# Performance work log

Measured on AMD Instinct MI355X. Metric: run time of the kernel, lower is better.

The kernel has to match this reference:

```python
import jax, jax.numpy as jnp
import numpy as np

B, C, L = 8, 1024, 4096
CTX = 768
NUM_GROUPS = 8
EPS = 1e-5
HEAD_DIM = C  # num_heads = 1 (only shape-consistent config of the module)


def setup_inputs() -> dict:
    key = jax.random.key(0)
    ks = jax.random.split(key, 8)
    s = 0.02
    return {
        "x": jax.random.normal(ks[0], (B, C, L), jnp.float32),
        "context": jax.random.normal(ks[1], (B, CTX), jnp.float32),
        "gn_gamma": jnp.ones((C,), jnp.float32),
        "gn_beta": jnp.zeros((C,), jnp.float32),
        "ln_gamma": jnp.ones((CTX,), jnp.float32),
        "ln_beta": jnp.zeros((CTX,), jnp.float32),
        "Wq": jax.random.normal(ks[2], (C, C), jnp.float32) * s,
        "bq": jnp.zeros((C,), jnp.float32),
        "Wkv": jax.random.normal(ks[3], (2 * C, CTX), jnp.float32) * s,
        "bkv": jnp.zeros((2 * C,), jnp.float32),
        "Wp": jax.random.normal(ks[4], (C, C), jnp.float32) * s,
        "bp": jnp.zeros((C,), jnp.float32),
    }


def group_norm(x, gamma, beta):
    # x: (B, C, L) -> normalize within each of NUM_GROUPS groups over (C//G, L)
    b, c, l = x.shape
    xg = x.reshape(b, NUM_GROUPS, c // NUM_GROUPS, l)
    mu = xg.mean(axis=(2, 3), keepdims=True)
    var = xg.var(axis=(2, 3), keepdims=True)
    xg = (xg - mu) * jax.lax.rsqrt(var + EPS)
    return xg.reshape(b, c, l) * gamma[None, :, None] + beta[None, :, None]


def layer_norm(x, gamma, beta):
    mu = x.mean(axis=-1, keepdims=True)
    var = x.var(axis=-1, keepdims=True)
    return (x - mu) * jax.lax.rsqrt(var + EPS) * gamma + beta


def reference(x, context, gn_gamma, gn_beta, ln_gamma, ln_beta,
              Wq, bq, Wkv, bkv, Wp, bp):
    residual = x
    xn = group_norm(x, gn_gamma, gn_beta)                   # (B, C, L)
    ctx = layer_norm(context, ln_gamma, ln_beta)            # (B, CTX)
    # 1x1 conv Q projection == channel GEMM
    q = jnp.einsum('bcl,oc->bol', xn, Wq) + bq[None, :, None]  # (B, C, L)
    kv = ctx @ Wkv.T + bkv                                  # (B, 2C)
    k, v = kv[:, :C], kv[:, C:]                             # each (B, C) = (B, head_dim)
    scale = HEAD_DIM ** (-0.5)
    # per-position score against the single context key; softmax over L
    attn = jax.nn.softmax(jnp.einsum('bcl,bc->bl', q, k) * scale, axis=-1)  # (B, L)
    # broadcast-weighted outer product (fused form of expand+mul+sum over heads=1)
    out = attn[:, None, :] * v[:, :, None]                  # (B, C, L)
    out = jnp.einsum('bcl,oc->bol', out, Wp) + bp[None, :, None]
    return residual + out
```

## Files before the change

kernel.cpp:

```cpp
#include <hip/hip_runtime.h>
#include <math.h>

#define NB   8
#define NC   1024
#define NL   4096
#define NCTX 768
#define EPSV 1e-5f
#define SCALEV 0.03125f

typedef float floatx4 __attribute__((ext_vector_type(4)));

enum : int {
  OFF_KV    = 0,
  OFF_PV    = 16384,
  OFF_QP    = 24576,
  OFF_SPART = 548864,
  OFF_TPART = 552960,
  OFF_ATTN  = 1077248,
  OFF_S     = 1110016,
  WS_FLOATS = 1110024
};

__device__ __forceinline__ float breduce_sum(float v, float* red) {
  int t = threadIdx.x;
  red[t] = v; __syncthreads();
  for (int s = 128; s > 0; s >>= 1) { if (t < s) red[t] += red[t + s]; __syncthreads(); }
  float r = red[0]; __syncthreads();
  return r;
}
__device__ __forceinline__ float wave_sum(float v) {
  #pragma unroll
  for (int off = 32; off > 0; off >>= 1) v += __shfl_xor(v, off, 64);
  return v;
}

__global__ void k_kv(const float* __restrict__ ctx, const float* __restrict__ lng,
                     const float* __restrict__ lnb, const float* __restrict__ Wkv,
                     const float* __restrict__ bkv, float* __restrict__ ws) {
  __shared__ __align__(16) float scf[8 * NCTX];
  int t = threadIdx.x, bid = blockIdx.x;
  int wave = t >> 6, lane = t & 63;
  if (bid == 0 && t < NB) ws[OFF_S + t] = 0.f;
  #pragma unroll
  for (int bb = 0; bb < 2; bb++) {
    int b = wave * 2 + bb;
    const float* row = ctx + b * NCTX;
    float v[12];
    float s = 0.f;
    #pragma unroll
    for (int k = 0; k < 12; k++) { v[k] = row[lane + 64 * k]; s += v[k]; }
    float mu = wave_sum(s) * (1.0f / NCTX);
    float s2 = 0.f;
    #pragma unroll
    for (int k = 0; k < 12; k++) { float d = v[k] - mu; s2 = fmaf(d, d, s2); }
    float rstd = rsqrtf(wave_sum(s2) * (1.0f / NCTX) + EPSV);
    #pragma unroll
    for (int k = 0; k < 12; k++) {
      int j = lane + 64 * k;
      scf[b * NCTX + j] = (v[k] - mu) * rstd * lng[j] + lnb[j];
    }
  }
  __syncthreads();
  const float4* W4 = reinterpret_cast<const float4*>(Wkv);
  const float4* sc4 = reinterpret_cast<const float4*>(scf);
  #pragma unroll
  for (int rr = 0; rr < 4; rr++) {
    int j = bid * 16 + wave * 4 + rr;
    float4 wv0 = W4[(size_t)j * 192 + lane];
    float4 wv1 = W4[(size_t)j * 192 + lane + 64];
    float4 wv2 = W4[(size_t)j * 192 + lane + 128];
    #pragma unroll
    for (int b = 0; b < 8; b++) {
      const float4* sb = sc4 + b * 192;
      float4 c0 = sb[lane], c1 = sb[lane + 64], c2 = sb[lane + 128];
      float a = wv0.x*c0.x + wv0.y*c0.y + wv0.z*c0.z + wv0.w*c0.w
              + wv1.x*c1.x + wv1.y*c1.y + wv1.z*c1.z + wv1.w*c1.w
              + wv2.x*c2.x + wv2.y*c2.y + wv2.z*c2.z + wv2.w*c2.w;
      a = wave_sum(a);
      if (lane == 0) ws[OFF_KV + b * 2048 + j] = a + bkv[j];
    }
  }
}

__global__ void k_mv(const float* __restrict__ Wq, const float* __restrict__ Wp,
                     float* __restrict__ ws) {
  __shared__ float4 sbuf[8 * 256];
  int t = threadIdx.x, bid = blockIdx.x;
  if (bid < 64) {
    float* sk = reinterpret_cast<float*>(sbuf);
    if (t < 128) { int b = t >> 4, o = t & 15; sk[b * 16 + o] = ws[OFF_KV + b * 2048 + bid * 16 + o]; }
    __syncthreads();
    const float4* Wq4 = reinterpret_cast<const float4*>(Wq);
    float4 acc[8];
    #pragma unroll
    for (int b = 0; b < 8; b++) acc[b] = make_float4(0.f, 0.f, 0.f, 0.f);
    int o0 = bid * 16;
    #pragma unroll 4
    for (int oi = 0; oi < 16; oi++) {
      float4 w = Wq4[(size_t)(o0 + oi) * 256 + t];
      #pragma unroll
      for (int b = 0; b < 8; b++) {
        float kk = sk[b * 16 + oi];
        acc[b].x = fmaf(kk, w.x, acc[b].x);
        acc[b].y = fmaf(kk, w.y, acc[b].y);
        acc[b].z = fmaf(kk, w.z, acc[b].z);
        acc[b].w = fmaf(kk, w.w, acc[b].w);
      }
    }
    float4* qp4 = reinterpret_cast<float4*>(ws + OFF_QP);
    #pragma unroll
    for (int b = 0; b < 8; b++) qp4[(bid * 8 + b) * 256 + t] = acc[b];
  } else {
    const float4* kv4 = reinterpret_cast<const float4*>(ws + OFF_KV);
    #pragma unroll
    for (int rep = 0; rep < 8; rep++) {
      int idx = rep * 256 + t;
      int b = idx >> 8, i = idx & 255;
      sbuf[idx] = kv4[b * 512 + 256 + i];
    }
    __syncthreads();
    int wave = t >> 6, lane = t & 63;
    const float4* Wp4 = reinterpret_cast<const float4*>(Wp);
    #pragma unroll
    for (int rr = 0; rr < 4; rr++) {
      int o = (bid - 64) * 16 + wave * 4 + rr;
      float4 wv0 = Wp4[(size_t)o * 256 + lane];
      float4 wv1 = Wp4[(size_t)o * 256 + lane + 64];
      float4 wv2 = Wp4[(size_t)o * 256 + lane + 128];
      float4 wv3 = Wp4[(size_t)o * 256 + lane + 192];
      #pragma unroll
      for (int b = 0; b < 8; b++) {
        const float4* sb = sbuf + b * 256;
        float4 c0 = sb[lane], c1 = sb[lane + 64], c2 = sb[lane + 128], c3 = sb[lane + 192];
        float a = wv0.x*c0.x + wv0.y*c0.y + wv0.z*c0.z + wv0.w*c0.w
                + wv1.x*c1.x + wv1.y*c1.y + wv1.z*c1.z + wv1.w*c1.w
                + wv2.x*c2.x + wv2.y*c2.y + wv2.z*c2.z + wv2.w*c2.w
                + wv3.x*c3.x + wv3.y*c3.y + wv3.z*c3.z + wv3.w*c3.w;
        a = wave_sum(a);
        if (lane == 0) ws[OFF_PV + b * NC + o] = a;
      }
    }
  }
}

__global__ void k_pass1(const float* __restrict__ x, const float* __restrict__ gng,
                        float* __restrict__ ws) {
  __shared__ float red[256];
  __shared__ float sw[64];
  __shared__ __align__(16) float4 part[192];
  int t  = threadIdx.x;
  int lc = blockIdx.x;
  int cs = blockIdx.y;
  int bz = blockIdx.z;
  int b = bz >> 3, g = bz & 7;
  int c0 = g * 128 + cs * 64;
  {
    int cl = t & 63, sp = t >> 6;
    const float* qp = ws + OFF_QP + b * 1024 + c0 + cl;
    float s = 0.f;
    #pragma unroll 4
    for (int oc = sp * 16; oc < sp * 16 + 16; oc++) s += qp[(size_t)oc * 8192];
    red[t] = s;
    __syncthreads();
    if (t < 64) sw[t] = gng[c0 + t] * ((red[t] + red[t + 64]) + (red[t + 128] + red[t + 192]));
    __syncthreads();
  }
  int tl = t & 63, q = t >> 6;
  int l4 = lc * 64 + tl;
  const float4* x4 = reinterpret_cast<const float4*>(x);
  float4 tacc = make_float4(0.f, 0.f, 0.f, 0.f);
  float s1 = 0.f, s2 = 0.f;
  #pragma unroll 4
  for (int ci = q * 16; ci < q * 16 + 16; ci++) {
    float w = sw[ci];
    float4 v = x4[(size_t)(b * NC + c0 + ci) * 1024 + l4];
    tacc.x = fmaf(w, v.x, tacc.x);
    tacc.y = fmaf(w, v.y, tacc.y);
    tacc.z = fmaf(w, v.z, tacc.z);
    tacc.w = fmaf(w, v.w, tacc.w);
    s1 += (v.x + v.y) + (v.z + v.w);
    s2 = fmaf(v.x, v.x, s2); s2 = fmaf(v.y, v.y, s2);
    s2 = fmaf(v.z, v.z, s2); s2 = fmaf(v.w, v.w, s2);
  }
  if (q > 0) part[(q - 1) * 64 + tl] = tacc;
  __syncthreads();
  if (q == 0) {
    float4 p0 = part[tl], p1 = part[64 + tl], p2 = part[128 + tl];
    tacc.x += (p0.x + p1.x) + p2.x;
    tacc.y += (p0.y + p1.y) + p2.y;
    tacc.z += (p0.z + p1.z) + p2.z;
    tacc.w += (p0.w + p1.w) + p2.w;
    reinterpret_cast<float4*>(ws + OFF_TPART)[(size_t)(bz * 2 + cs) * 1024 + l4] = tacc;
  }
  float S1 = breduce_sum(s1, red);
  float S2 = breduce_sum(s2, red);
  if (t == 0) {
    float* sp = ws + OFF_SPART + (bz * 32 + cs * 16 + lc) * 2;
    sp[0] = S1; sp[1] = S2;
  }
}

__global__ void k_scores(float* __restrict__ ws) {
  __shared__ float srstd[8];
  __shared__ float red[256];
  int t = threadIdx.x, lc = blockIdx.x, b = blockIdx.y;
  if (t < 8) {
    const float* sp = ws + OFF_SPART + (b * 8 + t) * 64;
    float S1 = 0.f, S2 = 0.f;
    #pragma unroll
    for (int i = 0; i < 32; i++) { S1 += sp[i * 2]; S2 += sp[i * 2 + 1]; }
    const float invN = 1.0f / (128.0f * (float)NL);
    float mu = S1 * invN;
    float var = S2 * invN - mu * mu;
    srstd[t] = rsqrtf(var + EPSV);
  }
  __syncthreads();
  float esum = 0.f;
  #pragma unroll
  for (int r = 0; r < 2; r++) {
    int l = lc * 512 + r * 256 + t;
    float acc = 0.f;
    #pragma unroll
    for (int g = 0; g < 8; g++) {
      const float* tg = ws + OFF_TPART + (size_t)(b * 8 + g) * 8192;
      acc = fmaf(srstd[g], tg[l] + tg[4096 + l], acc);
    }
    float e = expf(fminf(SCALEV * acc, 60.0f));
    ws[OFF_ATTN + b * NL + l] = e;
    esum += e;
  }
  float tot = breduce_sum(esum, red);
  if (t == 0) atomicAdd(ws + OFF_S + b, tot);
}

__global__ void k_out(const float* __restrict__ x, const float* __restrict__ bp,
                      const float* __restrict__ ws, float* __restrict__ out) {
  const float4* x4 = reinterpret_cast<const float4*>(x);
  floatx4* o4 = reinterpret_cast<floatx4*>(out);
  const float4* a4 = reinterpret_cast<const float4*>(ws + OFF_ATTN);
  const float* pv = ws + OFF_PV;
  const float* Ss = ws + OFF_S;
  const size_t NT4 = (size_t)NB * NC * NL / 4;
  for (size_t i = (size_t)blockIdx.x * blockDim.x + threadIdx.x; i < NT4;
       i += (size_t)gridDim.x * blockDim.x) {
    int b  = (int)(i >> 20);
    int c  = (int)((i >> 10) & (NC - 1));
    int l4 = (int)(i & 1023);
    float4 xv = x4[i];
    float4 av = a4[(size_t)b * 1024 + l4];
    float p  = pv[b * NC + c] / Ss[b];
    float bb = bp[c];
    floatx4 r;
    r.x = xv.x + fmaf(av.x, p, bb);
    r.y = xv.y + fmaf(av.y, p, bb);
    r.z = xv.z + fmaf(av.z, p, bb);
    r.w = xv.w + fmaf(av.w, p, bb);
    __builtin_nontemporal_store(r, &o4[i]);
  }
}

extern "C" void kernel_launch(void* const* d_in, const int* in_sizes, int n_in,
                              void* d_out, int out_size, void* d_ws, size_t ws_size,
                              hipStream_t stream) {
  const float* x    = (const float*)d_in[0];
  const float* ctx  = (const float*)d_in[1];
  const float* gng  = (const float*)d_in[2];
  const float* lng  = (const float*)d_in[4];
  const float* lnb  = (const float*)d_in[5];
  const float* Wq   = (const float*)d_in[6];
  const float* Wkv  = (const float*)d_in[8];
  const float* bkv  = (const float*)d_in[9];
  const float* Wp   = (const float*)d_in[10];
  const float* bp   = (const float*)d_in[11];
  float* ws  = (float*)d_ws;
  float* out = (float*)d_out;

  hipLaunchKernelGGL(k_kv,     dim3(128),        dim3(256), 0, stream, ctx, lng, lnb, Wkv, bkv, ws);
  hipLaunchKernelGGL(k_mv,     dim3(128),        dim3(256), 0, stream, Wq, Wp, ws);
  hipLaunchKernelGGL(k_pass1,  dim3(16, 2, 64),  dim3(256), 0, stream, x, gng, ws);
  hipLaunchKernelGGL(k_scores, dim3(8, 8),       dim3(256), 0, stream, ws);
  hipLaunchKernelGGL(k_out,    dim3(2048),       dim3(256), 0, stream, x, bp, ws, out);
}
```

Baseline: 101.2 us.

## Fuse KV and Q-fold into one head kernel, move Wp matvec into scores kernel

Merges the KV projection and the Wq fold into a single k_head launch. Blocks that own the first 1024 KV rows keep their k values in shared memory and immediately fold them through Wq, which removes the k_mv launch and its reread of KV from global memory. Extra blocks in k_head stream Wp through the cache as a prefetch whose result is discarded. The Wp·v matvec moves off the critical path into k_tail alongside the scores computation, which reduces the kernel count from five to four. The trade-off is that the Wq fold now waits on the KV compute inside the same block, and the Wp prefetch adds bandwidth that only helps if the lines stay in cache.

```diff
diff --git a/kernel.cpp b/kernel.cpp
--- a/kernel.cpp
+++ b/kernel.cpp
@@ -34,112 +34,91 @@
   return v;
 }
 
-__global__ void k_kv(const float* __restrict__ ctx, const float* __restrict__ lng,
-                     const float* __restrict__ lnb, const float* __restrict__ Wkv,
-                     const float* __restrict__ bkv, float* __restrict__ ws) {
+__global__ void k_head(const float* __restrict__ ctx, const float* __restrict__ lng,
+                       const float* __restrict__ lnb, const float* __restrict__ Wkv,
+                       const float* __restrict__ bkv, const float* __restrict__ Wq,
+                       const float* __restrict__ Wp,  float* __restrict__ ws) {
   __shared__ __align__(16) float scf[8 * NCTX];
+  __shared__ float sk[8 * 16];
   int t = threadIdx.x, bid = blockIdx.x;
   int wave = t >> 6, lane = t & 63;
   if (bid == 0 && t < NB) ws[OFF_S + t] = 0.f;
-  #pragma unroll
-  for (int bb = 0; bb < 2; bb++) {
-    int b = wave * 2 + bb;
-    const float* row = ctx + b * NCTX;
-    float v[12];
-    float s = 0.f;
-    #pragma unroll
-    for (int k = 0; k < 12; k++) { v[k] = row[lane + 64 * k]; s += v[k]; }
-    float mu = wave_sum(s) * (1.0f / NCTX);
-    float s2 = 0.f;
-    #pragma unroll
-    for (int k = 0; k < 12; k++) { float d = v[k] - mu; s2 = fmaf(d, d, s2); }
-    float rstd = rsqrtf(wave_sum(s2) * (1.0f / NCTX) + EPSV);
-    #pragma unroll
-    for (int k = 0; k < 12; k++) {
-      int j = lane + 64 * k;
-      scf[b * NCTX + j] = (v[k] - mu) * rstd * lng[j] + lnb[j];
-    }
-  }
-  __syncthreads();
-  const float4* W4 = reinterpret_cast<const float4*>(Wkv);
-  const float4* sc4 = reinterpret_cast<const float4*>(scf);
-  #pragma unroll
-  for (int rr = 0; rr < 4; rr++) {
-    int j = bid * 16 + wave * 4 + rr;
-    float4 wv0 = W4[(size_t)j * 192 + lane];
-    float4 wv1 = W4[(size_t)j * 192 + lane + 64];
-    float4 wv2 = W4[(size_t)j * 192 + lane + 128];
-    #pragma unroll
-    for (int b = 0; b < 8; b++) {
-      const float4* sb = sc4 + b * 192;
-      float4 c0 = sb[lane], c1 = sb[lane + 64], c2 = sb[lane + 128];
-      float a = wv0.x*c0.x + wv0.y*c0.y + wv0.z*c0.z + wv0.w*c0.w
-              + wv1.x*c1.x + wv1.y*c1.y + wv1.z*c1.z + wv1.w*c1.w
-              + wv2.x*c2.x + wv2.y*c2.y + wv2.z*c2.z + wv2.w*c2.w;
-      a = wave_sum(a);
-      if (lane == 0) ws[OFF_KV + b * 2048 + j] = a + bkv[j];
-    }
-  }
-}
-
-__global__ void k_mv(const float* __restrict__ Wq, const float* __restrict__ Wp,
-                     float* __restrict__ ws) {
-  __shared__ float4 sbuf[8 * 256];
-  int t = threadIdx.x, bid = blockIdx.x;
-  if (bid < 64) {
-    float* sk = reinterpret_cast<float*>(sbuf);
-    if (t < 128) { int b = t >> 4, o = t & 15; sk[b * 16 + o] = ws[OFF_KV + b * 2048 + bid * 16 + o]; }
-    __syncthreads();
-    const float4* Wq4 = reinterpret_cast<const float4*>(Wq);
-    float4 acc[8];
-    #pragma unroll
-    for (int b = 0; b < 8; b++) acc[b] = make_float4(0.f, 0.f, 0.f, 0.f);
-    int o0 = bid * 16;
-    #pragma unroll 4
-    for (int oi = 0; oi < 16; oi++) {
-      float4 w = Wq4[(size_t)(o0 + oi) * 256 + t];
+
+  if (bid < 128) {
+    #pragma unroll
+    for (int bb = 0; bb < 2; bb++) {
+      int b = wave * 2 + bb;
+      const float* row = ctx + b * NCTX;
+      float v[12];
+      float s = 0.f;
+      #pragma unroll
+      for (int k = 0; k < 12; k++) { v[k] = row[lane + 64 * k]; s += v[k]; }
+      float mu = wave_sum(s) * (1.0f / NCTX);
+      float s2 = 0.f;
+      #pragma unroll
+      for (int k = 0; k < 12; k++) { float d = v[k] - mu; s2 = fmaf(d, d, s2); }
+      float rstd = rsqrtf(wave_sum(s2) * (1.0f / NCTX) + EPSV);
+      #pragma unroll
+      for (int k = 0; k < 12; k++) {
+        int j = lane + 64 * k;
+        scf[b * NCTX + j] = (v[k] - mu) * rstd * lng[j] + lnb[j];
+      }
+    }
+    __syncthreads();
+    const float4* W4 = reinterpret_cast<const float4*>(Wkv);
+    const float4* sc4 = reinterpret_cast<const float4*>(scf);
+    #pragma unroll
+    for (int rr = 0; rr < 4; rr++) {
+      int j = bid * 16 + wave * 4 + rr;
+      float4 wv0 = W4[(size_t)j * 192 + lane];
+      float4 wv1 = W4[(size_t)j * 192 + lane + 64];
+      float4 wv2 = W4[(size_t)j * 192 + lane + 128];
       #pragma unroll
       for (int b = 0; b < 8; b++) {
-        float kk = sk[b * 16 + oi];
-        acc[b].x = fmaf(kk, w.x, acc[b].x);
-        acc[b].y = fmaf(kk, w.y, acc[b].y);
-        acc[b].z = fmaf(kk, w.z, acc[b].z);
-        acc[b].w = fmaf(kk, w.w, acc[b].w);
-      }
-    }
-    float4* qp4 = reinterpret_cast<float4*>(ws + OFF_QP);
-    #pragma unroll
-    for (int b = 0; b < 8; b++) qp4[(bid * 8 + b) * 256 + t] = acc[b];
-  } else {
-    const float4* kv4 = reinterpret_cast<const float4*>(ws + OFF_KV);
-    #pragma unroll
-    for (int rep = 0; rep < 8; rep++) {
-      int idx = rep * 256 + t;
-      int b = idx >> 8, i = idx & 255;
-      sbuf[idx] = kv4[b * 512 + 256 + i];
-    }
-    __syncthreads();
-    int wave = t >> 6, lane = t & 63;
-    const float4* Wp4 = reinterpret_cast<const float4*>(Wp);
-    #pragma unroll
-    for (int rr = 0; rr < 4; rr++) {
-      int o = (bid - 64) * 16 + wave * 4 + rr;
-      float4 wv0 = Wp4[(size_t)o * 256 + lane];
-      float4 wv1 = Wp4[(size_t)o * 256 + lane + 64];
-      float4 wv2 = Wp4[(size_t)o * 256 + lane + 128];
-      float4 wv3 = Wp4[(size_t)o * 256 + lane + 192];
-      #pragma unroll
-      for (int b = 0; b < 8; b++) {
-        const float4* sb = sbuf + b * 256;
-        float4 c0 = sb[lane], c1 = sb[lane + 64], c2 = sb[lane + 128], c3 = sb[lane + 192];
+        const float4* sb = sc4 + b * 192;
+        float4 c0 = sb[lane], c1 = sb[lane + 64], c2 = sb[lane + 128];
         float a = wv0.x*c0.x + wv0.y*c0.y + wv0.z*c0.z + wv0.w*c0.w
                 + wv1.x*c1.x + wv1.y*c1.y + wv1.z*c1.z + wv1.w*c1.w
-                + wv2.x*c2.x + wv2.y*c2.y + wv2.z*c2.z + wv2.w*c2.w
-                + wv3.x*c3.x + wv3.y*c3.y + wv3.z*c3.z + wv3.w*c3.w;
+                + wv2.x*c2.x + wv2.y*c2.y + wv2.z*c2.z + wv2.w*c2.w;
         a = wave_sum(a);
-        if (lane == 0) ws[OFF_PV + b * NC + o] = a;
-      }
-    }
+        if (lane == 0) {
+          ws[OFF_KV + b * 2048 + j] = a + bkv[j];
+          if (bid < 64) sk[b * 16 + (wave * 4 + rr)] = a + bkv[j];
+        }
+      }
+    }
+    if (bid < 64) {
+      __syncthreads();
+      const float4* Wq4 = reinterpret_cast<const float4*>(Wq);
+      float4 acc[8];
+      #pragma unroll
+      for (int b = 0; b < 8; b++) acc[b] = make_float4(0.f, 0.f, 0.f, 0.f);
+      int o0 = bid * 16;
+      #pragma unroll 4
+      for (int oi = 0; oi < 16; oi++) {
+        float4 w = Wq4[(size_t)(o0 + oi) * 256 + t];
+        #pragma unroll
+        for (int b = 0; b < 8; b++) {
+          float kk = sk[b * 16 + oi];
+          acc[b].x = fmaf(kk, w.x, acc[b].x);
+          acc[b].y = fmaf(kk, w.y, acc[b].y);
+          acc[b].z = fmaf(kk, w.z, acc[b].z);
+          acc[b].w = fmaf(kk, w.w, acc[b].w);
+        }
+      }
+      float4* qp4 = reinterpret_cast<float4*>(ws + OFF_QP);
+      #pragma unroll
+      for (int b = 0; b < 8; b++) qp4[(bid * 8 + b) * 256 + t] = acc[b];
+    }
+  } else {
+    const float4* Wp4 = reinterpret_cast<const float4*>(Wp);
+    int pid = bid - 128;
+    float acc = 0.f;
+    for (int idx = pid * 256 + t; idx < 262144; idx += 128 * 256) {
+      float4 v = Wp4[idx];
+      acc += v.x + v.y + v.z + v.w;
+    }
+    asm volatile("" :: "v"(acc));
   }
 }
 
@@ -200,37 +179,72 @@
   }
 }
 
-__global__ void k_scores(float* __restrict__ ws) {
-  __shared__ float srstd[8];
-  __shared__ float red[256];
-  int t = threadIdx.x, lc = blockIdx.x, b = blockIdx.y;
-  if (t < 8) {
-    const float* sp = ws + OFF_SPART + (b * 8 + t) * 64;
-    float S1 = 0.f, S2 = 0.f;
-    #pragma unroll
-    for (int i = 0; i < 32; i++) { S1 += sp[i * 2]; S2 += sp[i * 2 + 1]; }
-    const float invN = 1.0f / (128.0f * (float)NL);
-    float mu = S1 * invN;
-    float var = S2 * invN - mu * mu;
-    srstd[t] = rsqrtf(var + EPSV);
-  }
-  __syncthreads();
-  float esum = 0.f;
-  #pragma unroll
-  for (int r = 0; r < 2; r++) {
-    int l = lc * 512 + r * 256 + t;
-    float acc = 0.f;
-    #pragma unroll
-    for (int g = 0; g < 8; g++) {
-      const float* tg = ws + OFF_TPART + (size_t)(b * 8 + g) * 8192;
-      acc = fmaf(srstd[g], tg[l] + tg[4096 + l], acc);
-    }
-    float e = expf(fminf(SCALEV * acc, 60.0f));
-    ws[OFF_ATTN + b * NL + l] = e;
-    esum += e;
-  }
-  float tot = breduce_sum(esum, red);
-  if (t == 0) atomicAdd(ws + OFF_S + b, tot);
+__global__ void k_tail(const float* __restrict__ Wp, float* __restrict__ ws) {
+  __shared__ __align__(16) char smem[32768];
+  int t = threadIdx.x, bid = blockIdx.x;
+  if (bid < 64) {
+    float* srstd = (float*)smem;
+    float* red   = (float*)(smem + 1024);
+    int lc = bid & 7, b = bid >> 3;
+    if (t < 8) {
+      const float* sp = ws + OFF_SPART + (b * 8 + t) * 64;
+      float S1 = 0.f, S2 = 0.f;
+      #pragma unroll
+      for (int i = 0; i < 32; i++) { S1 += sp[i * 2]; S2 += sp[i * 2 + 1]; }
+      const float invN = 1.0f / (128.0f * (float)NL);
+      float mu = S1 * invN;
+      float var = S2 * invN - mu * mu;
+      srstd[t] = rsqrtf(var + EPSV);
+    }
+    __syncthreads();
+    float esum = 0.f;
+    #pragma unroll
+    for (int r = 0; r < 2; r++) {
+      int l = lc * 512 + r * 256 + t;
+      float acc = 0.f;
+      #pragma unroll
+      for (int g = 0; g < 8; g++) {
+        const float* tg = ws + OFF_TPART + (size_t)(b * 8 + g) * 8192;
+        acc = fmaf(srstd[g], tg[l] + tg[4096 + l], acc);
+      }
+      float e = expf(fminf(SCALEV * acc, 60.0f));
+      ws[OFF_ATTN + b * NL + l] = e;
+      esum += e;
+    }
+    float tot = breduce_sum(esum, red);
+    if (t == 0) atomicAdd(ws + OFF_S + b, tot);
+  } else {
+    float4* sbuf = (float4*)smem;
+    const float4* kv4 = reinterpret_cast<const float4*>(ws + OFF_KV);
+    #pragma unroll
+    for (int rep = 0; rep < 8; rep++) {
+      int idx = rep * 256 + t;
+      int b = idx >> 8, i = idx & 255;
+      sbuf[idx] = kv4[b * 512 + 256 + i];
+    }
+    __syncthreads();
+    int wave = t >> 6, lane = t & 63;
+    const float4* Wp4 = reinterpret_cast<const float4*>(Wp);
+    #pragma unroll
+    for (int rr = 0; rr < 2; rr++) {
+      int o = (bid - 64) * 8 + wave * 2 + rr;
+      float4 w0 = Wp4[(size_t)o * 256 + lane];
+      float4 w1 = Wp4[(size_t)o * 256 + lane + 64];
+      float4 w2 = Wp4[(size_t)o * 256 + lane + 128];
+      float4 w3 = Wp4[(size_t)o * 256 + lane + 192];
+      #pragma unroll
+      for (int b = 0; b < 8; b++) {
+        const float4* sb = sbuf + b * 256;
+        float4 c0 = sb[lane], c1 = sb[lane + 64], c2 = sb[lane + 128], c3 = sb[lane + 192];
+        float a = w0.x*c0.x + w0.y*c0.y + w0.z*c0.z + w0.w*c0.w
+                + w1.x*c1.x + w1.y*c1.y + w1.z*c1.z + w1.w*c1.w
+                + w2.x*c2.x + w2.y*c2.y + w2.z*c2.z + w2.w*c2.w
+                + w3.x*c3.x + w3.y*c3.y + w3.z*c3.z + w3.w*c3.w;
+        a = wave_sum(a);
+        if (lane == 0) ws[OFF_PV + b * NC + o] = a;
+      }
+    }
+  }
 }
 
 __global__ void k_out(const float* __restrict__ x, const float* __restrict__ bp,
@@ -275,9 +289,8 @@
   float* ws  = (float*)d_ws;
   float* out = (float*)d_out;
 
-  hipLaunchKernelGGL(k_kv,     dim3(128),        dim3(256), 0, stream, ctx, lng, lnb, Wkv, bkv, ws);
-  hipLaunchKernelGGL(k_mv,     dim3(128),        dim3(256), 0, stream, Wq, Wp, ws);
+  hipLaunchKernelGGL(k_head,   dim3(256),        dim3(256), 0, stream, ctx, lng, lnb, Wkv, bkv, Wq, Wp, ws);
   hipLaunchKernelGGL(k_pass1,  dim3(16, 2, 64),  dim3(256), 0, stream, x, gng, ws);
-  hipLaunchKernelGGL(k_scores, dim3(8, 8),       dim3(256), 0, stream, ws);
+  hipLaunchKernelGGL(k_tail,   dim3(192),        dim3(256), 0, stream, Wp, ws);
   hipLaunchKernelGGL(k_out,    dim3(2048),       dim3(256), 0, stream, x, bp, ws, out);
 }
```

After: 94.93 us, median of 2. 6.2% less time.
